# Kernel tuning notes

Hardware: AMD Instinct MI355X
Metric: run time of the kernel (lower is better)

## Reference

```python
import jax, jax.numpy as jnp
import numpy as np

N = 50000       # nodes
E = 800000      # edges (avg degree 16)
D = 64          # node_size
ES = 16         # edge_size = num_edge_types + 1
R = 3           # rounds_of_propagation
HG = 2 * D      # hG_size
MSG = 2 * D + ES  # 144


def setup_inputs() -> dict:
    key = jax.random.key(0)
    ks = jax.random.split(key, 20)
    s = 0.05
    return {
        "node_vectors": jax.random.normal(ks[0], (N, D), jnp.float32),
        "edge_vectors": jax.random.normal(ks[1], (E, ES), jnp.float32),
        "Wef": jax.random.normal(ks[2], (R, 2 * D, MSG), jnp.float32) * s,
        "bef": jnp.zeros((R, 2 * D), jnp.float32),
        "Wer": jax.random.normal(ks[3], (R, 2 * D, MSG), jnp.float32) * s,
        "ber": jnp.zeros((R, 2 * D), jnp.float32),
        "W_ih": jax.random.normal(ks[4], (R, 3 * D, 2 * D), jnp.float32) * s,
        "W_hh": jax.random.normal(ks[5], (R, 3 * D, D), jnp.float32) * s,
        "b_ih": jnp.zeros((R, 3 * D), jnp.float32),
        "b_hh": jnp.zeros((R, 3 * D), jnp.float32),
        "W_fm": jax.random.normal(ks[6], (HG, D), jnp.float32) * s,
        "b_fm": jnp.zeros((HG,), jnp.float32),
        "W_gm": jax.random.normal(ks[7], (HG, D), jnp.float32) * s,
        "b_gm": jnp.zeros((HG,), jnp.float32),
        "W_dec": jax.random.normal(ks[8], (1, HG + D), jnp.float32) * s,
        "b_dec": jnp.zeros((1,), jnp.float32),
        "u_indices": jax.random.randint(ks[9], (E,), 0, N, jnp.int32),
        "v_indices": jax.random.randint(ks[10], (E,), 0, N, jnp.int32),
        "target_idx": 0,
    }


def reference(node_vectors, edge_vectors, Wef, bef, Wer, ber, W_ih, W_hh,
              b_ih, b_hh, W_fm, b_fm, W_gm, b_gm, W_dec, b_dec,
              u_indices, v_indices, target_idx):
    n_nodes = node_vectors.shape[0]
    h = node_vectors
    for i in range(Wef.shape[0]):
        # gather endpoint features + edge features -> [E, MSG]
        raw = jnp.concatenate([h[u_indices], h[v_indices], edge_vectors], axis=1)
        msg_f = raw @ Wef[i].T + bef[i]   # [E, 2D]
        msg_r = raw @ Wer[i].T + ber[i]   # [E, 2D]
        # node.incoming -> edges where node is v; node.outgoing -> node is u
        agg = (jax.ops.segment_sum(msg_f, v_indices, num_segments=n_nodes)
               + jax.ops.segment_sum(msg_r, u_indices, num_segments=n_nodes))
        # torch GRUCell(agg, h)
        gi = agg @ W_ih[i].T + b_ih[i]
        gh = h @ W_hh[i].T + b_hh[i]
        i_r, i_z, i_n = jnp.split(gi, 3, axis=1)
        h_r, h_z, h_n = jnp.split(gh, 3, axis=1)
        r = jax.nn.sigmoid(i_r + h_r)
        z = jax.nn.sigmoid(i_z + h_z)
        n = jnp.tanh(i_n + r * h_n)
        h = (1.0 - z) * n + z * h
    # gated graph aggregation -> h_G [1, HG]
    h_G = jnp.sum((h @ W_fm.T + b_fm) * jax.nn.sigmoid(h @ W_gm.T + b_gm),
                  axis=0, keepdims=True)
    # add-edge decision logit
    feat = jnp.concatenate([h_G, h[target_idx][None, :]], axis=1)
    return feat @ W_dec.T + b_dec  # [1, 1]
```

## Files before the change

### kernel.cpp

```cpp
#include <hip/hip_runtime.h>
#include <math.h>

#define D64 64
#define ES16 16
#define NB5 256

typedef unsigned short u16;
typedef _Float16 half8 __attribute__((ext_vector_type(8)));
typedef __attribute__((ext_vector_type(4))) float f32x4;


__device__ __forceinline__ float sigf(float x){ return 1.0f/(1.0f + __expf(-x)); }
__device__ __forceinline__ float tanhfast(float x){ return 2.0f*sigf(2.0f*x) - 1.0f; }
__device__ __forceinline__ u16 f2h(float f){
  _Float16 h = (_Float16)f;
  u16 r; __builtin_memcpy(&r, &h, 2); return r;
}
__device__ __forceinline__ float h2f(u16 b){
  _Float16 h; __builtin_memcpy(&h, &b, 2); return (float)h;
}
__device__ __forceinline__ float2 up2(unsigned w){
  _Float16 lo, hi;
  u16 a = (u16)(w & 0xFFFF), b = (u16)(w >> 16);
  __builtin_memcpy(&lo, &a, 2); __builtin_memcpy(&hi, &b, 2);
  return make_float2((float)lo, (float)hi);
}

__global__ void k_count(const int* __restrict__ u, const int* __restrict__ v,
                        int* __restrict__ cnt, int* __restrict__ rin,
                        int* __restrict__ rout, int N, int E){
  int e = blockIdx.x*256 + threadIdx.x;
  if(e < E){
    rin[e]  = atomicAdd(&cnt[v[e]], 1);
    rout[e] = atomicAdd(&cnt[N + u[e]], 1);
  }
}

__global__ void k_scan1(const int* __restrict__ cnt, int* __restrict__ part, int M){
  __shared__ int sm[256];
  int i = blockIdx.x*256 + threadIdx.x;
  sm[threadIdx.x] = (i < M) ? cnt[i] : 0;
  __syncthreads();
  for(int s = 128; s > 0; s >>= 1){
    if(threadIdx.x < s) sm[threadIdx.x] += sm[threadIdx.x + s];
    __syncthreads();
  }
  if(threadIdx.x == 0) part[blockIdx.x] = sm[0];
}

__global__ void k_scan2(int* __restrict__ part, int nb){
  __shared__ int sm[1024];
  int t = threadIdx.x;
  int orig = (t < nb) ? part[t] : 0;
  sm[t] = orig;
  __syncthreads();
  for(int off = 1; off < 1024; off <<= 1){
    int add = (t >= off) ? sm[t - off] : 0;
    __syncthreads();
    sm[t] += add;
    __syncthreads();
  }
  if(t < nb) part[t] = sm[t] - orig;
}

__global__ void k_scan3(int* __restrict__ cnt, const int* __restrict__ part,
                        int M, int total){
  __shared__ int sm[256];
  int t = threadIdx.x;
  int i = blockIdx.x*256 + t;
  int orig = (i < M) ? cnt[i] : 0;
  sm[t] = orig;
  __syncthreads();
  for(int off = 1; off < 256; off <<= 1){
    int add = (t >= off) ? sm[t - off] : 0;
    __syncthreads();
    sm[t] += add;
    __syncthreads();
  }
  if(i < M) cnt[i] = part[blockIdx.x] + sm[t] - orig;
  if(i == 0) cnt[M] = total;
}

__global__ void k_fill2(const int* __restrict__ u, const int* __restrict__ v,
                        const int* __restrict__ off, const int* __restrict__ rin,
                        const int* __restrict__ rout, int* __restrict__ rows,
                        int* __restrict__ srcs, int N, int E){
  int e = blockIdx.x*256 + threadIdx.x;
  if(e < E){
    int uu = u[e], vv = v[e];
    int p = off[vv] + rin[e];
    int q = off[N + uu] + rout[e];
    rows[p] = e; srcs[p] = uu;
    rows[q] = e; srcs[q] = vv;
  }
}

__global__ void k_cvt16(const float* __restrict__ src, u16* __restrict__ dst, int total){
  int i = blockIdx.x*256 + threadIdx.x;
  if(i < total) dst[i] = f2h(src[i]);
}

__global__ void k_einout(const float* __restrict__ ev, const int* __restrict__ off,
                         const int* __restrict__ rows,
                         float* __restrict__ Ein, float* __restrict__ Eout, int N){
  int n = (blockIdx.x*blockDim.x + threadIdx.x) >> 6;
  int lane = threadIdx.x & 63;
  if(n >= N) return;
  int t = lane & 15, s = lane >> 4;
  {
    float a0 = 0.f, a1 = 0.f;
    int p = off[n] + s, p1 = off[n+1];
    for(; p + 4 < p1; p += 8){
      a0 += ev[rows[p]*ES16 + t];
      a1 += ev[rows[p+4]*ES16 + t];
    }
    if(p < p1) a0 += ev[rows[p]*ES16 + t];
    float a = a0 + a1;
    a += __shfl_xor(a, 16, 64);
    a += __shfl_xor(a, 32, 64);
    if(lane < 16) Ein[n*ES16 + lane] = a;
  }
  {
    float b0 = 0.f, b1 = 0.f;
    int p = off[N+n] + s, p1 = off[N+n+1];
    for(; p + 4 < p1; p += 8){
      b0 += ev[rows[p]*ES16 + t];
      b1 += ev[rows[p+4]*ES16 + t];
    }
    if(p < p1) b0 += ev[rows[p]*ES16 + t];
    float b = b0 + b1;
    b += __shfl_xor(b, 16, 64);
    b += __shfl_xor(b, 32, 64);
    if(lane < 16) Eout[n*ES16 + lane] = b;
  }
}

__global__ void k_aggr(const u16* __restrict__ h16, const int* __restrict__ off,
                       const int* __restrict__ srcs,
                       u16* __restrict__ Sin16, u16* __restrict__ Sout16, int N){
  int n = (blockIdx.x*blockDim.x + threadIdx.x) >> 6;
  int lane = threadIdx.x & 63;
  if(n >= N) return;
  const int half = lane >> 5;
  const int fl   = lane & 31;
  const int gw   = half ? (N + n) : n;
  int p  = off[gw], p1 = off[gw+1];
  const unsigned* hsrc = (const unsigned*)h16;
  float sx0 = 0.f, sy0 = 0.f, sx1 = 0.f, sy1 = 0.f;
  for(; p + 8 <= p1; p += 8){
    int s0 = srcs[p],   s1 = srcs[p+1], s2 = srcs[p+2], s3 = srcs[p+3];
    int s4 = srcs[p+4], s5 = srcs[p+5], s6 = srcs[p+6], s7 = srcs[p+7];
    unsigned w0 = hsrc[(size_t)s0*32 + fl];
    unsigned w1 = hsrc[(size_t)s1*32 + fl];
    unsigned w2 = hsrc[(size_t)s2*32 + fl];
    unsigned w3 = hsrc[(size_t)s3*32 + fl];
    unsigned w4 = hsrc[(size_t)s4*32 + fl];
    unsigned w5 = hsrc[(size_t)s5*32 + fl];
    unsigned w6 = hsrc[(size_t)s6*32 + fl];
    unsigned w7 = hsrc[(size_t)s7*32 + fl];
    float2 f0 = up2(w0), f1 = up2(w1), f2 = up2(w2), f3 = up2(w3);
    float2 f4 = up2(w4), f5 = up2(w5), f6 = up2(w6), f7 = up2(w7);
    sx0 += (f0.x + f1.x) + (f4.x + f5.x);
    sy0 += (f0.y + f1.y) + (f4.y + f5.y);
    sx1 += (f2.x + f3.x) + (f6.x + f7.x);
    sy1 += (f2.y + f3.y) + (f6.y + f7.y);
  }
  for(; p + 4 <= p1; p += 4){
    int s0 = srcs[p], s1 = srcs[p+1], s2 = srcs[p+2], s3 = srcs[p+3];
    unsigned w0 = hsrc[(size_t)s0*32 + fl];
    unsigned w1 = hsrc[(size_t)s1*32 + fl];
    unsigned w2 = hsrc[(size_t)s2*32 + fl];
    unsigned w3 = hsrc[(size_t)s3*32 + fl];
    float2 f0 = up2(w0), f1 = up2(w1), f2 = up2(w2), f3 = up2(w3);
    sx0 += f0.x + f1.x; sy0 += f0.y + f1.y;
    sx1 += f2.x + f3.x; sy1 += f2.y + f3.y;
  }
  for(; p < p1; ++p){
    float2 f0 = up2(hsrc[(size_t)srcs[p]*32 + fl]);
    sx0 += f0.x; sy0 += f0.y;
  }
  unsigned pw = (unsigned)f2h(sx0 + sx1) | ((unsigned)f2h(sy0 + sy1) << 16);
  unsigned* dst = half ? (unsigned*)Sout16 : (unsigned*)Sin16;
  dst[(size_t)n*32 + fl] = pw;
}

__global__ void k_preA(const float* __restrict__ Wef, const float* __restrict__ bef,
                       const float* __restrict__ Wer, const float* __restrict__ ber,
                       u16* __restrict__ bA){
  int b = blockIdx.x;
  int r = b / 80, t = b % 80;
  int nt = t / 10, kt = t % 10;
  int lane = threadIdx.x;
  int j = nt*16 + (lane & 15);
  int ks0 = kt*32 + (lane >> 4)*8;
  const float* wef = Wef + (size_t)r*128*144;
  const float* wer = Wer + (size_t)r*128*144;
  u16 v[8];
  #pragma unroll
  for(int e = 0; e < 8; ++e){
    int ks = ks0 + e;
    float val;
    if(ks < 144)       val = wef[j*144 + ks];
    else if(ks == 144) val = bef[r*128 + j];
    else if(ks < 160)  val = 0.f;
    else if(ks < 304)  val = wer[j*144 + (ks - 160)];
    else if(ks == 304) val = ber[r*128 + j];
    else               val = 0.f;
    v[e] = f2h(val);
  }
  u16* dst = bA + ((size_t)b*64 + lane)*8;
  #pragma unroll
  for(int e = 0; e < 8; ++e) dst[e] = v[e];
}

__global__ void k_preB(const float* __restrict__ Wih, const float* __restrict__ Whh,
                       const float* __restrict__ bih, const float* __restrict__ bhh,
                       u16* __restrict__ bB){
  int b = blockIdx.x;
  int r = b / 96, t = b % 96;
  int nt = t / 8, kt = t % 8;
  int lane = threadIdx.x;
  int q = nt*16 + (lane & 15);
  int ks0 = kt*32 + (lane >> 4)*8;
  const float* wih = Wih + (size_t)r*192*128;
  const float* whh = Whh + (size_t)r*192*64;
  u16 v[8];
  #pragma unroll
  for(int e = 0; e < 8; ++e){
    int ks = ks0 + e;
    float val;
    if(ks < 128)       val = wih[q*128 + ks];
    else if(ks == 128) val = bih[r*192 + q];
    else if(ks < 160)  val = 0.f;
    else if(ks < 224)  val = whh[q*64 + (ks - 160)];
    else if(ks == 224) val = bhh[r*192 + q];
    else               val = 0.f;
    v[e] = f2h(val);
  }
  u16* dst = bB + ((size_t)b*64 + lane)*8;
  #pragma unroll
  for(int e = 0; e < 8; ++e) dst[e] = v[e];
}

__global__ void k_preC(const float* __restrict__ Wfm, const float* __restrict__ Wgm,
                       u16* __restrict__ bC){
  int b = blockIdx.x;
  int nt = b >> 2, kt = (b >> 1) & 1, fg = b & 1;
  int lane = threadIdx.x;
  int j = nt*16 + (lane & 15);
  int ks0 = kt*32 + (lane >> 4)*8;
  const float* W = fg ? Wgm : Wfm;
  u16 v[8];
  #pragma unroll
  for(int e = 0; e < 8; ++e) v[e] = f2h(W[j*64 + ks0 + e]);
  u16* dst = bC + ((size_t)b*64 + lane)*8;
  #pragma unroll
  for(int e = 0; e < 8; ++e) dst[e] = v[e];
}

__global__ __launch_bounds__(512) void k34_mfma(
    const u16* __restrict__ h16, const u16* __restrict__ Sin16,
    const u16* __restrict__ Sout16, const float* __restrict__ Ein,
    const float* __restrict__ Eout, const int* __restrict__ off,
    const u16* __restrict__ bA, const u16* __restrict__ bB,
    u16* __restrict__ h16next, int N){
  __shared__ u16 xA[64][328];
  __shared__ u16 x2[64][264];
  const int lane = threadIdx.x & 63;
  const int wv   = __builtin_amdgcn_readfirstlane(threadIdx.x >> 6);
  const int base = blockIdx.x * 64;

  for(int ii = 0; ii < 8; ++ii){
    int i = wv*8 + ii;
    int n = base + i; if(n >= N) n = N - 1;
    float fi = (float)(off[n+1] - off[n]);
    float fo = (float)(off[N+n+1] - off[N+n]);
    u16 hv16 = h16[(size_t)n*D64 + lane];
    float hv = h2f(hv16);
    xA[i][lane]        = Sin16[(size_t)n*D64 + lane];
    xA[i][64 + lane]   = f2h(fi*hv);
    xA[i][160 + lane]  = f2h(fo*hv);
    xA[i][224 + lane]  = Sout16[(size_t)n*D64 + lane];
    x2[i][160 + lane]  = hv16;
    if(lane < 16){
      xA[i][128 + lane] = f2h(Ein[(size_t)n*ES16 + lane]);
      xA[i][288 + lane] = f2h(Eout[(size_t)n*ES16 + lane]);
    }
    if(lane == 0){
      xA[i][144] = f2h(fi); xA[i][304] = f2h(fo);
      x2[i][128] = 0x3C00;  x2[i][224] = 0x3C00;
    }
    if(lane >= 1 && lane < 16){ xA[i][144 + lane] = 0; xA[i][304 + lane] = 0; }
    if(lane >= 1 && lane < 32){ x2[i][128 + lane] = 0; x2[i][224 + lane] = 0; }
  }
  __syncthreads();

  half8 bw[10];
  #pragma unroll
  for(int kt = 0; kt < 10; ++kt)
    bw[kt] = *(const half8*)(bA + ((size_t)(wv*10 + kt)*64 + lane)*8);

  f32x4 accA[4];
  const int arow = lane & 15;
  const int akof = (lane >> 4) * 8;
  #pragma unroll
  for(int m = 0; m < 4; ++m){
    f32x4 a = {0.f, 0.f, 0.f, 0.f};
    #pragma unroll
    for(int kt = 0; kt < 10; ++kt){
      half8 av = *(const half8*)&xA[m*16 + arow][kt*32 + akof];
      a = __builtin_amdgcn_mfma_f32_16x16x32_f16(av, bw[kt], a, 0, 0, 0);
    }
    accA[m] = a;
  }

  const int jb = wv * 16;
  #pragma unroll
  for(int m = 0; m < 4; ++m){
    #pragma unroll
    for(int reg = 0; reg < 4; ++reg){
      int nl = m*16 + (lane >> 4)*4 + reg;
      x2[nl][jb + (lane & 15)] = f2h(accA[m][reg]);
    }
  }
  __syncthreads();

  #pragma unroll
  for(int uu = 0; uu < 2; ++uu){
    const int unit = wv*2 + uu;
    const int mt  = unit >> 2;
    const int tri = unit & 3;
    f32x4 aR  = {0.f,0.f,0.f,0.f};
    f32x4 aZ  = {0.f,0.f,0.f,0.f};
    f32x4 aNi = {0.f,0.f,0.f,0.f};
    f32x4 aNh = {0.f,0.f,0.f,0.f};
    #pragma unroll
    for(int kt = 0; kt < 8; ++kt){
      half8 av = *(const half8*)&x2[mt*16 + arow][kt*32 + akof];
      half8 bR = *(const half8*)(bB + ((size_t)((tri    )*8 + kt)*64 + lane)*8);
      half8 bZ = *(const half8*)(bB + ((size_t)((tri + 4)*8 + kt)*64 + lane)*8);
      half8 bN = *(const half8*)(bB + ((size_t)((tri + 8)*8 + kt)*64 + lane)*8);
      aR = __builtin_amdgcn_mfma_f32_16x16x32_f16(av, bR, aR, 0, 0, 0);
      aZ = __builtin_amdgcn_mfma_f32_16x16x32_f16(av, bZ, aZ, 0, 0, 0);
      if(kt < 5) aNi = __builtin_amdgcn_mfma_f32_16x16x32_f16(av, bN, aNi, 0, 0, 0);
      else       aNh = __builtin_amdgcn_mfma_f32_16x16x32_f16(av, bN, aNh, 0, 0, 0);
    }
    const int q = tri*16 + (lane & 15);
    #pragma unroll
    for(int reg = 0; reg < 4; ++reg){
      int node = base + mt*16 + (lane >> 4)*4 + reg;
      float r  = sigf(aR[reg]);
      float z  = sigf(aZ[reg]);
      float nn = tanhfast(aNi[reg] + r*aNh[reg]);
      if(node < N){
        float hq = h2f(h16[(size_t)node*D64 + q]);
        h16next[(size_t)node*D64 + q] = f2h((1.f - z)*nn + z*hq);
      }
    }
  }
}

__global__ __launch_bounds__(512) void k5m(
    const u16* __restrict__ h16, const u16* __restrict__ bC,
    const float* __restrict__ bfm, const float* __restrict__ bgm,
    float* __restrict__ partials, int N, int nT){
  __shared__ u16 xh[64][72];
  const int lane = threadIdx.x & 63;
  const int wv   = __builtin_amdgcn_readfirstlane(threadIdx.x >> 6);
  const int arow = lane & 15;
  const int akof = (lane >> 4) * 8;
  half8 bF[2], bG[2];
  #pragma unroll
  for(int kt = 0; kt < 2; ++kt){
    bF[kt] = *(const half8*)(bC + ((size_t)(wv*4 + kt*2 + 0)*64 + lane)*8);
    bG[kt] = *(const half8*)(bC + ((size_t)(wv*4 + kt*2 + 1)*64 + lane)*8);
  }
  const float fb = bfm[wv*16 + arow];
  const float gb = bgm[wv*16 + arow];
  float acc = 0.f;
  for(int tile = blockIdx.x; tile < nT; tile += NB5){
    const int base = tile * 64;
    __syncthreads();
    for(int ii = 0; ii < 8; ++ii){
      int i = wv*8 + ii;
      int n = base + i;
      xh[i][lane] = (n < N) ? h16[(size_t)n*D64 + lane] : (u16)0;
    }
    __syncthreads();
    #pragma unroll
    for(int m = 0; m < 4; ++m){
      f32x4 F = {0.f,0.f,0.f,0.f};
      f32x4 G = {0.f,0.f,0.f,0.f};
      #pragma unroll
      for(int kt = 0; kt < 2; ++kt){
        half8 av = *(const half8*)&xh[m*16 + arow][kt*32 + akof];
        F = __builtin_amdgcn_mfma_f32_16x16x32_f16(av, bF[kt], F, 0, 0, 0);
        G = __builtin_amdgcn_mfma_f32_16x16x32_f16(av, bG[kt], G, 0, 0, 0);
      }
      #pragma unroll
      for(int reg = 0; reg < 4; ++reg){
        int node = base + m*16 + (lane >> 4)*4 + reg;
        if(node < N)
          acc += (F[reg] + fb) * sigf(G[reg] + gb);
      }
    }
  }
  acc += __shfl_xor(acc, 16, 64);
  acc += __shfl_xor(acc, 32, 64);
  if(lane < 16) partials[blockIdx.x*128 + wv*16 + lane] = acc;
}

__global__ void k6_dec(const float* __restrict__ partials, int nb,
                       const u16* __restrict__ h16,
                       const float* __restrict__ Wdec, const float* __restrict__ bdec,
                       const int* __restrict__ tgt, float* __restrict__ out){
  __shared__ float sm[256];
  int t = threadIdx.x;
  float v = 0.f;
  if(t < 128){
    float s0 = 0.f, s1 = 0.f, s2 = 0.f, s3 = 0.f;
    for(int b = 0; b + 4 <= nb; b += 4){
      s0 += partials[(b+0)*128 + t];
      s1 += partials[(b+1)*128 + t];
      s2 += partials[(b+2)*128 + t];
      s3 += partials[(b+3)*128 + t];
    }
    v = ((s0 + s1) + (s2 + s3)) * Wdec[t];
  } else if(t < 192){
    v = h2f(h16[(size_t)tgt[0]*D64 + (t - 128)]) * Wdec[t];
  }
  sm[t] = v;
  __syncthreads();
  for(int s = 128; s > 0; s >>= 1){
    if(t < s) sm[t] += sm[t + s];
    __syncthreads();
  }
  if(t == 0) out[0] = sm[0] + bdec[0];
}

extern "C" void kernel_launch(void* const* d_in, const int* in_sizes, int n_in,
                              void* d_out, int out_size, void* d_ws, size_t ws_size,
                              hipStream_t stream){
  const float* nodev = (const float*)d_in[0];
  const float* ev    = (const float*)d_in[1];
  const float* Wef   = (const float*)d_in[2];
  const float* bef   = (const float*)d_in[3];
  const float* Wer   = (const float*)d_in[4];
  const float* ber   = (const float*)d_in[5];
  const float* Wih   = (const float*)d_in[6];
  const float* Whh   = (const float*)d_in[7];
  const float* bih   = (const float*)d_in[8];
  const float* bhh   = (const float*)d_in[9];
  const float* Wfm   = (const float*)d_in[10];
  const float* bfm   = (const float*)d_in[11];
  const float* Wgm   = (const float*)d_in[12];
  const float* bgm   = (const float*)d_in[13];
  const float* Wdec  = (const float*)d_in[14];
  const float* bdec  = (const float*)d_in[15];
  const int* uidx    = (const int*)d_in[16];
  const int* vidx    = (const int*)d_in[17];
  const int* tgt     = (const int*)d_in[18];

  const int N = in_sizes[0] / 64;
  const int E = in_sizes[16];
  const int R = in_sizes[2] / (128*144);

  char* w = (char*)d_ws;
  auto alloc = [&](size_t bytes) -> void* {
    void* p = (void*)w;
    w += (bytes + 255) & ~(size_t)255;
    return p;
  };
  int* off       = (int*)alloc(((size_t)2*N + 1) * 4);
  int* rin       = (int*)alloc((size_t)E * 4);
  int* rout      = (int*)alloc((size_t)E * 4);
  int* rows      = (int*)alloc((size_t)2*E * 4);
  int* srcs      = (int*)alloc((size_t)2*E * 4);
  int* part      = (int*)alloc(4096 * 4);
  float* Ein     = (float*)alloc((size_t)N*16*4);
  float* Eout    = (float*)alloc((size_t)N*16*4);
  u16* Sin16     = (u16*)alloc((size_t)N*64*2);
  u16* Sout16    = (u16*)alloc((size_t)N*64*2);
  u16* g0        = (u16*)alloc((size_t)N*64*2);
  u16* gA        = (u16*)alloc((size_t)N*64*2);
  u16* gB        = (u16*)alloc((size_t)N*64*2);
  u16* bA        = (u16*)alloc((size_t)R*80*64*8*2);
  u16* bB        = (u16*)alloc((size_t)R*96*64*8*2);
  u16* bC        = (u16*)alloc((size_t)32*64*8*2);
  float* partial = (float*)alloc((size_t)NB5*128*4);

  hipMemsetAsync(off, 0, ((size_t)2*N+1)*4, stream);

  int eb = (E + 255)/256;
  k_count<<<eb, 256, 0, stream>>>(uidx, vidx, off, rin, rout, N, E);
  int M = 2*N;
  int nb = (M + 255)/256;
  k_scan1<<<nb, 256, 0, stream>>>(off, part, M);
  k_scan2<<<1, 1024, 0, stream>>>(part, nb);
  k_scan3<<<nb, 256, 0, stream>>>(off, part, M, 2*E);
  k_fill2<<<eb, 256, 0, stream>>>(uidx, vidx, off, rin, rout, rows, srcs, N, E);
  int wb = (N + 3)/4;
  k_einout<<<wb, 256, 0, stream>>>(ev, off, rows, Ein, Eout, N);
  k_cvt16<<<(N*64 + 255)/256, 256, 0, stream>>>(nodev, g0, N*64);

  k_preA<<<R*80, 64, 0, stream>>>(Wef, bef, Wer, ber, bA);
  k_preB<<<R*96, 64, 0, stream>>>(Wih, Whh, bih, bhh, bB);
  k_preC<<<32, 64, 0, stream>>>(Wfm, Wgm, bC);

  int nT = (N + 63)/64;
  const u16* g16cur = g0;
  u16* gbufs[2] = {gA, gB};
  for(int r = 0; r < R; ++r){
    k_aggr<<<wb, 256, 0, stream>>>(g16cur, off, srcs, Sin16, Sout16, N);
    u16* gn = gbufs[r & 1];
    k34_mfma<<<nT, 512, 0, stream>>>(g16cur, Sin16, Sout16, Ein, Eout, off,
                                     bA + (size_t)r*80*64*8,
                                     bB + (size_t)r*96*64*8,
                                     gn, N);
    g16cur = gn;
  }
  k5m<<<NB5, 512, 0, stream>>>(g16cur, bC, bfm, bgm, partial, N, nT);
  k6_dec<<<1, 256, 0, stream>>>(partial, NB5, g16cur, Wdec, bdec, tgt, (float*)d_out);
}
```

Before: 421.3 us.

## Pack degree counters into 16-bit halves, merge weight-prep kernels, deepen gather unroll

```diff
diff --git a/kernel.cpp b/kernel.cpp
--- a/kernel.cpp
+++ b/kernel.cpp
@@ -27,13 +27,22 @@
 }
 
 __global__ void k_count(const int* __restrict__ u, const int* __restrict__ v,
-                        int* __restrict__ cnt, int* __restrict__ rin,
+                        unsigned* __restrict__ cntp, int* __restrict__ rin,
                         int* __restrict__ rout, int N, int E){
   int e = blockIdx.x*256 + threadIdx.x;
   if(e < E){
-    rin[e]  = atomicAdd(&cnt[v[e]], 1);
-    rout[e] = atomicAdd(&cnt[N + u[e]], 1);
-  }
+    int kv = v[e];
+    int ku = N + u[e];
+    unsigned rv = atomicAdd(&cntp[kv >> 1], 1u << (16*(kv & 1)));
+    unsigned ru = atomicAdd(&cntp[ku >> 1], 1u << (16*(ku & 1)));
+    rin[e]  = (int)((rv >> (16*(kv & 1))) & 0xFFFFu);
+    rout[e] = (int)((ru >> (16*(ku & 1))) & 0xFFFFu);
+  }
+}
+
+__global__ void k_unpack(const unsigned* __restrict__ cntp, int* __restrict__ cnt, int M){
+  int i = blockIdx.x*256 + threadIdx.x;
+  if(i < M) cnt[i] = (int)((cntp[i >> 1] >> (16*(i & 1))) & 0xFFFFu);
 }
 
 __global__ void k_scan1(const int* __restrict__ cnt, int* __restrict__ part, int M){
@@ -147,6 +156,19 @@
   int p  = off[gw], p1 = off[gw+1];
   const unsigned* hsrc = (const unsigned*)h16;
   float sx0 = 0.f, sy0 = 0.f, sx1 = 0.f, sy1 = 0.f;
+  for(; p + 16 <= p1; p += 16){
+    int s[16]; unsigned w[16];
+    #pragma unroll
+    for(int j = 0; j < 16; ++j) s[j] = srcs[p + j];
+    #pragma unroll
+    for(int j = 0; j < 16; ++j) w[j] = hsrc[(size_t)s[j]*32 + fl];
+    #pragma unroll
+    for(int j = 0; j < 16; j += 4){
+      float2 f0 = up2(w[j]), f1 = up2(w[j+1]), f2 = up2(w[j+2]), f3 = up2(w[j+3]);
+      sx0 += f0.x + f1.x; sy0 += f0.y + f1.y;
+      sx1 += f2.x + f3.x; sy1 += f2.y + f3.y;
+    }
+  }
   for(; p + 8 <= p1; p += 8){
     int s0 = srcs[p],   s1 = srcs[p+1], s2 = srcs[p+2], s3 = srcs[p+3];
     int s4 = srcs[p+4], s5 = srcs[p+5], s6 = srcs[p+6], s7 = srcs[p+7];
@@ -184,78 +206,70 @@
   dst[(size_t)n*32 + fl] = pw;
 }
 
-__global__ void k_preA(const float* __restrict__ Wef, const float* __restrict__ bef,
-                       const float* __restrict__ Wer, const float* __restrict__ ber,
-                       u16* __restrict__ bA){
+__global__ void k_pre(const float* __restrict__ Wef, const float* __restrict__ bef,
+                      const float* __restrict__ Wer, const float* __restrict__ ber,
+                      const float* __restrict__ Wih, const float* __restrict__ Whh,
+                      const float* __restrict__ bih, const float* __restrict__ bhh,
+                      const float* __restrict__ Wfm, const float* __restrict__ Wgm,
+                      u16* __restrict__ bA, u16* __restrict__ bB,
+                      u16* __restrict__ bC, int R){
   int b = blockIdx.x;
-  int r = b / 80, t = b % 80;
-  int nt = t / 10, kt = t % 10;
   int lane = threadIdx.x;
-  int j = nt*16 + (lane & 15);
-  int ks0 = kt*32 + (lane >> 4)*8;
-  const float* wef = Wef + (size_t)r*128*144;
-  const float* wer = Wer + (size_t)r*128*144;
-  u16 v[8];
+  u16 val8[8];
+  u16* dst;
+  if(b < R*80){
+    int r = b / 80, t = b % 80;
+    int nt = t / 10, kt = t % 10;
+    int j = nt*16 + (lane & 15);
+    int ks0 = kt*32 + (lane >> 4)*8;
+    const float* wef = Wef + (size_t)r*128*144;
+    const float* wer = Wer + (size_t)r*128*144;
+    #pragma unroll
+    for(int e = 0; e < 8; ++e){
+      int ks = ks0 + e;
+      float val;
+      if(ks < 144)       val = wef[j*144 + ks];
+      else if(ks == 144) val = bef[r*128 + j];
+      else if(ks < 160)  val = 0.f;
+      else if(ks < 304)  val = wer[j*144 + (ks - 160)];
+      else if(ks == 304) val = ber[r*128 + j];
+      else               val = 0.f;
+      val8[e] = f2h(val);
+    }
+    dst = bA + ((size_t)b*64 + lane)*8;
+  } else if(b < R*80 + R*96){
+    int bb = b - R*80;
+    int r = bb / 96, t = bb % 96;
+    int nt = t / 8, kt = t % 8;
+    int q = nt*16 + (lane & 15);
+    int ks0 = kt*32 + (lane >> 4)*8;
+    const float* wih = Wih + (size_t)r*192*128;
+    const float* whh = Whh + (size_t)r*192*64;
+    #pragma unroll
+    for(int e = 0; e < 8; ++e){
+      int ks = ks0 + e;
+      float val;
+      if(ks < 128)       val = wih[q*128 + ks];
+      else if(ks == 128) val = bih[r*192 + q];
+      else if(ks < 160)  val = 0.f;
+      else if(ks < 224)  val = whh[q*64 + (ks - 160)];
+      else if(ks == 224) val = bhh[r*192 + q];
+      else               val = 0.f;
+      val8[e] = f2h(val);
+    }
+    dst = bB + ((size_t)bb*64 + lane)*8;
+  } else {
+    int bb = b - R*80 - R*96;
+    int nt = bb >> 2, kt = (bb >> 1) & 1, fg = bb & 1;
+    int j = nt*16 + (lane & 15);
+    int ks0 = kt*32 + (lane >> 4)*8;
+    const float* W = fg ? Wgm : Wfm;
+    #pragma unroll
+    for(int e = 0; e < 8; ++e) val8[e] = f2h(W[j*64 + ks0 + e]);
+    dst = bC + ((size_t)bb*64 + lane)*8;
+  }
   #pragma unroll
-  for(int e = 0; e < 8; ++e){
-    int ks = ks0 + e;
-    float val;
-    if(ks < 144)       val = wef[j*144 + ks];
-    else if(ks == 144) val = bef[r*128 + j];
-    else if(ks < 160)  val = 0.f;
-    else if(ks < 304)  val = wer[j*144 + (ks - 160)];
-    else if(ks == 304) val = ber[r*128 + j];
-    else               val = 0.f;
-    v[e] = f2h(val);
-  }
-  u16* dst = bA + ((size_t)b*64 + lane)*8;
-  #pragma unroll
-  for(int e = 0; e < 8; ++e) dst[e] = v[e];
-}
-
-__global__ void k_preB(const float* __restrict__ Wih, const float* __restrict__ Whh,
-                       const float* __restrict__ bih, const float* __restrict__ bhh,
-                       u16* __restrict__ bB){
-  int b = blockIdx.x;
-  int r = b / 96, t = b % 96;
-  int nt = t / 8, kt = t % 8;
-  int lane = threadIdx.x;
-  int q = nt*16 + (lane & 15);
-  int ks0 = kt*32 + (lane >> 4)*8;
-  const float* wih = Wih + (size_t)r*192*128;
-  const float* whh = Whh + (size_t)r*192*64;
-  u16 v[8];
-  #pragma unroll
-  for(int e = 0; e < 8; ++e){
-    int ks = ks0 + e;
-    float val;
-    if(ks < 128)       val = wih[q*128 + ks];
-    else if(ks == 128) val = bih[r*192 + q];
-    else if(ks < 160)  val = 0.f;
-    else if(ks < 224)  val = whh[q*64 + (ks - 160)];
-    else if(ks == 224) val = bhh[r*192 + q];
-    else               val = 0.f;
-    v[e] = f2h(val);
-  }
-  u16* dst = bB + ((size_t)b*64 + lane)*8;
-  #pragma unroll
-  for(int e = 0; e < 8; ++e) dst[e] = v[e];
-}
-
-__global__ void k_preC(const float* __restrict__ Wfm, const float* __restrict__ Wgm,
-                       u16* __restrict__ bC){
-  int b = blockIdx.x;
-  int nt = b >> 2, kt = (b >> 1) & 1, fg = b & 1;
-  int lane = threadIdx.x;
-  int j = nt*16 + (lane & 15);
-  int ks0 = kt*32 + (lane >> 4)*8;
-  const float* W = fg ? Wgm : Wfm;
-  u16 v[8];
-  #pragma unroll
-  for(int e = 0; e < 8; ++e) v[e] = f2h(W[j*64 + ks0 + e]);
-  u16* dst = bC + ((size_t)b*64 + lane)*8;
-  #pragma unroll
-  for(int e = 0; e < 8; ++e) dst[e] = v[e];
+  for(int e = 0; e < 8; ++e) dst[e] = val8[e];
 }
 
 __global__ __launch_bounds__(512) void k34_mfma(
@@ -471,6 +485,7 @@
     w += (bytes + 255) & ~(size_t)255;
     return p;
   };
+  unsigned* cntp = (unsigned*)alloc(((size_t)N + 1) * 4);
   int* off       = (int*)alloc(((size_t)2*N + 1) * 4);
   int* rin       = (int*)alloc((size_t)E * 4);
   int* rout      = (int*)alloc((size_t)E * 4);
@@ -489,12 +504,13 @@
   u16* bC        = (u16*)alloc((size_t)32*64*8*2);
   float* partial = (float*)alloc((size_t)NB5*128*4);
 
-  hipMemsetAsync(off, 0, ((size_t)2*N+1)*4, stream);
+  hipMemsetAsync(cntp, 0, ((size_t)N+1)*4, stream);
 
   int eb = (E + 255)/256;
-  k_count<<<eb, 256, 0, stream>>>(uidx, vidx, off, rin, rout, N, E);
+  k_count<<<eb, 256, 0, stream>>>(uidx, vidx, cntp, rin, rout, N, E);
   int M = 2*N;
   int nb = (M + 255)/256;
+  k_unpack<<<nb, 256, 0, stream>>>(cntp, off, M);
   k_scan1<<<nb, 256, 0, stream>>>(off, part, M);
   k_scan2<<<1, 1024, 0, stream>>>(part, nb);
   k_scan3<<<nb, 256, 0, stream>>>(off, part, M, 2*E);
@@ -503,9 +519,8 @@
   k_einout<<<wb, 256, 0, stream>>>(ev, off, rows, Ein, Eout, N);
   k_cvt16<<<(N*64 + 255)/256, 256, 0, stream>>>(nodev, g0, N*64);
 
-  k_preA<<<R*80, 64, 0, stream>>>(Wef, bef, Wer, ber, bA);
-  k_preB<<<R*96, 64, 0, stream>>>(Wih, Whh, bih, bhh, bB);
-  k_preC<<<32, 64, 0, stream>>>(Wfm, Wgm, bC);
+  k_pre<<<R*80 + R*96 + 32, 64, 0, stream>>>(Wef, bef, Wer, ber, Wih, Whh,
+                                             bih, bhh, Wfm, Wgm, bA, bB, bC, R);
 
   int nT = (N + 63)/64;
   const u16* g16cur = g0;
```

Result: no change. 422.4 us (+0.3%).
